# Kernel optimization log

Measured on AMD Instinct MI355X. Metric: run time of the kernel, lower is better.

Reference implementation:

```python
import jax, jax.numpy as jnp
import numpy as np
from jax import lax

BN_EPS = 1e-5
STRIDE = 1
PAD = 1  # autopad(3, d=1) = 1
DIL = 1
GROUPS = 1


def setup_inputs() -> dict:
    key = jax.random.key(0)
    ks = jax.random.split(key, 4)
    b, cin, h, w = 16, 256, 56, 56
    E, cout, k = 8, 256, 3
    x = jax.random.normal(ks[0], (b, cin, h, w), dtype=jnp.float32)
    routing_w = jax.random.normal(ks[1], (E, cin), dtype=jnp.float32) * (1.0 / np.sqrt(cin))
    routing_b = jax.random.normal(ks[2], (E,), dtype=jnp.float32) * 0.01
    # kaiming_normal fan_out: std = sqrt(2 / (cout * k * k))
    kw_std = np.sqrt(2.0 / (cout * k * k)).astype(np.float32)
    kernel_weights = jax.random.normal(ks[3], (E, cout, cin // GROUPS, k, k), dtype=jnp.float32) * kw_std
    bn_gamma = jnp.ones((cout,), dtype=jnp.float32)
    bn_beta = jnp.zeros((cout,), dtype=jnp.float32)
    bn_mean = jnp.zeros((cout,), dtype=jnp.float32)
    bn_var = jnp.ones((cout,), dtype=jnp.float32)
    return {"x": x, "routing_w": routing_w, "routing_b": routing_b,
            "kernel_weights": kernel_weights, "bn_gamma": bn_gamma,
            "bn_beta": bn_beta, "bn_mean": bn_mean, "bn_var": bn_var}


def reference(x, routing_w, routing_b, kernel_weights, bn_gamma, bn_beta, bn_mean, bn_var):
    # Routing: sigmoid(Linear(GAP(x)))  -> (b, E)
    pooled = x.mean(axis=(2, 3))                                   # (b, cin)
    r = jax.nn.sigmoid(pooled @ routing_w.T + routing_b)           # (b, E)
    # Per-sample combined kernels: sum_e r[b,e] * W[e]  -> (b, cout, cin, k, k)
    cw = jnp.einsum('be,eoihw->boihw', r, kernel_weights)
    # Per-sample conv (equivalent to the grouped conv with groups=b trick)
    def conv1(xi, wi):
        # xi: (cin, H, W), wi: (cout, cin, k, k)
        return lax.conv_general_dilated(
            xi[None], wi,
            window_strides=(STRIDE, STRIDE),
            padding=((PAD, PAD), (PAD, PAD)),
            rhs_dilation=(DIL, DIL),
            dimension_numbers=('NCHW', 'OIHW', 'NCHW'),
            feature_group_count=GROUPS)[0]
    y = jax.vmap(conv1)(x, cw)                                     # (b, cout, H, W)
    # BatchNorm (inference form) + SiLU
    inv = bn_gamma / jnp.sqrt(bn_var + BN_EPS)
    y = y * inv[None, :, None, None] + (bn_beta - bn_mean * inv)[None, :, None, None]
    return jax.nn.silu(y)
```

## Files before the change

kernel.cpp:

```cpp
#include <hip/hip_runtime.h>
#include <hip/hip_bf16.h>

typedef unsigned short u16;
typedef __attribute__((ext_vector_type(8))) short s16x8;
typedef __attribute__((ext_vector_type(4))) float f32x4;
typedef __attribute__((address_space(3))) u16 lds_u16;
typedef __attribute__((address_space(1))) const u16 g_u16;

#define CIN 256
#define COUT 256
#define NPIX 3136
#define CWROW 168
#define CWPB (16 * COUT * CWROW)

__device__ __forceinline__ u16 f2b(float f) {
  union { float f; unsigned u; } c; c.f = f;
  unsigned r = (c.u + 0x7FFFu + ((c.u >> 16) & 1u)) >> 16;
  return (u16)r;
}

__global__ __launch_bounds__(256)
void transpose_gap_kernel(const float* __restrict__ x, u16* __restrict__ xq,
                          float* __restrict__ pooled) {
  const int hg = blockIdx.x, ck = blockIdx.y, b = blockIdx.z;
  const int tid = threadIdx.x;
  const int ci = tid >> 4, sub = tid & 15;
  __shared__ __align__(16) u16 tile[928 * 8];

  if (tid < 32) {
    int r = tid >> 2, c4 = tid & 3;
    int u = r * 116 + (c4 < 2 ? c4 : 112 + c4);
    int us = u ^ ((u >> 3) & 7);
    *(uint4*)&tile[us * 8] = (uint4){0, 0, 0, 0};
  }

  const float* src = x + ((size_t)(b * CIN + ck * 16 + ci) * NPIX + (size_t)hg * 448);
  float s = 0.f;
#pragma unroll
  for (int it = 0; it < 7; ++it) {
    int p = it * 16 + sub;
    int row = p / 14, wq = p - row * 14;
    float4 v = *(const float4*)(src + p * 4);
    s += v.x + v.y + v.z + v.w;
    u16 q[4] = { f2b(v.x), f2b(v.y), f2b(v.z), f2b(v.w) };
#pragma unroll
    for (int k = 0; k < 4; ++k) {
      int wp = wq * 4 + 1 + k;
      int u = (row * 58 + wp) * 2 + (ci >> 3);
      int us = u ^ ((u >> 3) & 7);
      tile[us * 8 + (ci & 7)] = q[k];
    }
  }
  for (int off = 8; off; off >>= 1) s += __shfl_down(s, off, 16);
  if (sub == 0) atomicAdd(&pooled[b * CIN + ck * 16 + ci], s);

  __syncthreads();
  uint4* dst = (uint4*)(xq + ((size_t)(b * 16 + ck) * 58 + hg * 8 + 1) * 928);
  for (int idx = tid; idx < 928; idx += 256) {
    int us = idx ^ ((idx >> 3) & 7);
    dst[idx] = *(const uint4*)&tile[us * 8];
  }
  if (hg == 0 && tid < 116)
    ((uint4*)(xq + ((size_t)(b * 16 + ck) * 58) * 928))[tid] = (uint4){0, 0, 0, 0};
  if (hg == 6 && tid < 116)
    ((uint4*)(xq + ((size_t)(b * 16 + ck) * 58 + 57) * 928))[tid] = (uint4){0, 0, 0, 0};
}

__global__ __launch_bounds__(256)
void combine_kernel(const float* __restrict__ W, const float* __restrict__ pooled,
                    const float* __restrict__ rw, const float* __restrict__ rb,
                    u16* __restrict__ cw) {
  const int o = blockIdx.x, tid = threadIdx.x;
  __shared__ float rs[128];
  __shared__ __align__(16) u16 st[2][16 * CWROW];

  for (int i = tid; i < 672; i += 256) ((uint4*)st)[i] = (uint4){0, 0, 0, 0};

  if (tid < 128) {
    int b = tid >> 3, e = tid & 7;
    float s = rb[e];
    const float* pb = pooled + b * CIN;
    const float* we = rw + e * CIN;
    for (int c = 0; c < CIN; ++c) s += (pb[c] * (1.f / 3136.f)) * we[c];
    rs[tid] = 1.f / (1.f + __expf(-s));
  }
  float wreg[8][9];
#pragma unroll
  for (int e = 0; e < 8; ++e) {
    const float* wp = W + ((size_t)(e * COUT + o)) * 2304 + tid;
#pragma unroll
    for (int k = 0; k < 9; ++k) wreg[e][k] = wp[k * 256];
  }
  int slot[9];
#pragma unroll
  for (int k = 0; k < 9; ++k) {
    int j = tid + k * 256, ci = j / 9, t = j - ci * 9;
    slot[k] = (ci >> 4) * CWROW + t * 16 + (ci & 15);
  }
  __syncthreads();
  for (int b = 0; b < 16; ++b) {
    u16* sb = st[b & 1];
    float rv[8];
#pragma unroll
    for (int e = 0; e < 8; ++e) rv[e] = rs[b * 8 + e];
#pragma unroll
    for (int k = 0; k < 9; ++k) {
      float a = 0.f;
#pragma unroll
      for (int e = 0; e < 8; ++e) a += rv[e] * wreg[e][k];
      sb[slot[k]] = f2b(a);
    }
    __syncthreads();
    u16* dstb = cw + (size_t)b * CWPB;
    for (int i = tid; i < 336; i += 256) {
      int ck = i / 21, q = i - ck * 21;
      *(uint4*)(dstb + ck * (256 * CWROW) + o * CWROW + q * 8) =
          *(const uint4*)(sb + ck * CWROW + q * 8);
    }
  }
}

__global__ __launch_bounds__(256)
void conv_kernel(const u16* __restrict__ xq, const u16* __restrict__ cw,
                 const float* __restrict__ bng, const float* __restrict__ bnb,
                 const float* __restrict__ bnm, const float* __restrict__ bnv,
                 float* __restrict__ out) {
  const int l = blockIdx.x;
  const int xcd = l & 7, s = l >> 3;
  const int bb = (s >= 28) ? 1 : 0;
  const int b = xcd + 8 * bb;
  const int r = s - 28 * bb;
  const int ob = r / 7;
  const int o0 = ob * 64, h0 = (r - ob * 7) * 8;
  const int tid = threadIdx.x;
  const int wv = tid >> 6, lane = tid & 63, quad = lane >> 4, ln = lane & 15;

  __shared__ __align__(16) u16 xs[2][19 * 512];
  __shared__ __align__(16) u16 as_[2][64 * CWROW];

  f32x4 acc[4][7];
#pragma unroll
  for (int ms = 0; ms < 4; ++ms)
#pragma unroll
    for (int ns = 0; ns < 7; ++ns) acc[ms][ns] = (f32x4){0.f, 0.f, 0.f, 0.f};

  int bsite[7];
#pragma unroll
  for (int ns = 0; ns < 7; ++ns) {
    int pi = ns * 16 + ln;
    int hr = (pi >= 56) ? 1 : 0;
    int wc = pi - hr * 56;
    bsite[ns] = ((2 * wv + hr) * 58 + wc) * 16;
  }

  auto STAGE = [&](int ck, int buf) {
    const u16* xsrc = xq + ((size_t)(b * 16 + ck) * 58 + h0) * 928;
    const u16* asrc = cw + (size_t)b * CWPB + ((size_t)ck * COUT + o0) * CWROW;
    for (int g = wv; g < 40; g += 4) {
      if (g < 19)
        __builtin_amdgcn_global_load_lds((g_u16*)(xsrc + g * 512 + lane * 8),
                                         (lds_u16*)(&xs[buf][g * 512]), 16, 0, 0);
      else
        __builtin_amdgcn_global_load_lds((g_u16*)(asrc + (g - 19) * 512 + lane * 8),
                                         (lds_u16*)(&as_[buf][(g - 19) * 512]), 16, 0, 0);
    }
  };

  auto COMPUTE = [&](int buf) {
#pragma unroll
    for (int tp = 0; tp < 5; ++tp) {
      int t = tp * 2 + (quad >> 1);
      int dy, dx;
      if (t < 9) { dy = t / 3; dx = t - dy * 3; } else { dy = 1; dx = 1; }
      const int boff = (dy * 58 + dx) * 16 + (quad & 1) * 8;
      s16x8 af[4];
#pragma unroll
      for (int ms = 0; ms < 4; ++ms)
        af[ms] = *(const s16x8*)&as_[buf][(ms * 16 + ln) * CWROW + tp * 32 + quad * 8];
#pragma unroll
      for (int ns = 0; ns < 7; ++ns) {
        s16x8 bfr = *(const s16x8*)&xs[buf][bsite[ns] + boff];
#pragma unroll
        for (int ms = 0; ms < 4; ++ms)
          acc[ms][ns] = __builtin_amdgcn_mfma_f32_16x16x32_bf16(af[ms], bfr, acc[ms][ns], 0, 0, 0);
      }
    }
  };

  STAGE(0, 0);
  __syncthreads();
  for (int ck = 0; ck < 16; ck += 2) {
    STAGE(ck + 1, 1);
    COMPUTE(0);
    __syncthreads();
    if (ck < 14) STAGE(ck + 2, 0);
    COMPUTE(1);
    __syncthreads();
  }

#pragma unroll
  for (int ms = 0; ms < 4; ++ms) {
#pragma unroll
    for (int rr = 0; rr < 4; ++rr) {
      int o = o0 + ms * 16 + quad * 4 + rr;
      float inv = bng[o] * rsqrtf(bnv[o] + 1e-5f);
      float bias = bnb[o] - bnm[o] * inv;
      float* obp = out + ((size_t)(b * COUT + o)) * NPIX;
#pragma unroll
      for (int ns = 0; ns < 7; ++ns) {
        int pi = ns * 16 + ln;
        int hr = (pi >= 56) ? 1 : 0;
        int wc = pi - hr * 56;
        int hg = h0 + 2 * wv + hr;
        float v = acc[ms][ns][rr] * inv + bias;
        v = v / (1.f + __expf(-v));
        obp[hg * 56 + wc] = v;
      }
    }
  }
}

extern "C" void kernel_launch(void* const* d_in, const int* in_sizes, int n_in,
                              void* d_out, int out_size, void* d_ws, size_t ws_size,
                              hipStream_t stream) {
  const float* x   = (const float*)d_in[0];
  const float* rw  = (const float*)d_in[1];
  const float* rb  = (const float*)d_in[2];
  const float* W   = (const float*)d_in[3];
  const float* bng = (const float*)d_in[4];
  const float* bnb = (const float*)d_in[5];
  const float* bnm = (const float*)d_in[6];
  const float* bnv = (const float*)d_in[7];
  float* out = (float*)d_out;

  char* wsb = (char*)d_ws;
  u16*  cw     = (u16*)wsb;
  u16*  xq     = (u16*)(wsb + 22020096);
  float* pooled = (float*)(wsb + 22020096 + 27558912);

  hipMemsetAsync(pooled, 0, 16 * CIN * sizeof(float), stream);
  transpose_gap_kernel<<<dim3(7, 16, 16), 256, 0, stream>>>(x, xq, pooled);
  combine_kernel<<<256, 256, 0, stream>>>(W, pooled, rw, rb, cw);
  conv_kernel<<<dim3(448), 256, 0, stream>>>(xq, cw, bng, bnb, bnm, bnv, out);
}
```

Measured before the change: 233.4 us.

## Retile conv to 14-row blocks with triple-buffered pipeline and drop GAP atomics

The conv kernel now uses 256 blocks of 448 threads (7 waves), each covering 14 output rows and 64 output channels. It triple-buffers LDS stages with explicit vmcnt waits, raw barriers and raised MFMA priority, so loads are issued two chunks ahead. The GAP reduction writes per-row-group partial sums that combine_kernel adds up in LDS, which removes the atomics and the memset launch. Per-tap offsets are also hoisted out of the compute loop. The larger LDS footprint and single-block occupancy risk worse latency hiding.

```diff
diff --git a/kernel.cpp b/kernel.cpp
--- a/kernel.cpp
+++ b/kernel.cpp
@@ -21,7 +21,7 @@
 
 __global__ __launch_bounds__(256)
 void transpose_gap_kernel(const float* __restrict__ x, u16* __restrict__ xq,
-                          float* __restrict__ pooled) {
+                          float* __restrict__ parts) {
   const int hg = blockIdx.x, ck = blockIdx.y, b = blockIdx.z;
   const int tid = threadIdx.x;
   const int ci = tid >> 4, sub = tid & 15;
@@ -33,7 +33,6 @@
     int us = u ^ ((u >> 3) & 7);
     *(uint4*)&tile[us * 8] = (uint4){0, 0, 0, 0};
   }
-
   const float* src = x + ((size_t)(b * CIN + ck * 16 + ci) * NPIX + (size_t)hg * 448);
   float s = 0.f;
 #pragma unroll
@@ -52,8 +51,7 @@
     }
   }
   for (int off = 8; off; off >>= 1) s += __shfl_down(s, off, 16);
-  if (sub == 0) atomicAdd(&pooled[b * CIN + ck * 16 + ci], s);
-
+  if (sub == 0) parts[(hg * 16 + b) * 256 + ck * 16 + ci] = s;
   __syncthreads();
   uint4* dst = (uint4*)(xq + ((size_t)(b * 16 + ck) * 58 + hg * 8 + 1) * 928);
   for (int idx = tid; idx < 928; idx += 256) {
@@ -67,19 +65,26 @@
 }
 
 __global__ __launch_bounds__(256)
-void combine_kernel(const float* __restrict__ W, const float* __restrict__ pooled,
+void combine_kernel(const float* __restrict__ W, const float* __restrict__ parts,
                     const float* __restrict__ rw, const float* __restrict__ rb,
                     u16* __restrict__ cw) {
   const int o = blockIdx.x, tid = threadIdx.x;
+  __shared__ float pooled_lds[16 * 256];
   __shared__ float rs[128];
   __shared__ __align__(16) u16 st[2][16 * CWROW];
-
-  for (int i = tid; i < 672; i += 256) ((uint4*)st)[i] = (uint4){0, 0, 0, 0};
-
+  for (int b = 0; b < 16; ++b) {
+    float s = 0.f;
+#pragma unroll
+    for (int hg = 0; hg < 7; ++hg) s += parts[(hg * 16 + b) * 256 + tid];
+    pooled_lds[b * 256 + tid] = s;
+  }
+  for (int i = tid; i < (2 * 16 * CWROW) / 8; i += 256)
+    ((uint4*)st)[i] = (uint4){0, 0, 0, 0};
+  __syncthreads();
   if (tid < 128) {
     int b = tid >> 3, e = tid & 7;
     float s = rb[e];
-    const float* pb = pooled + b * CIN;
+    const float* pb = pooled_lds + b * 256;
     const float* we = rw + e * CIN;
     for (int c = 0; c < CIN; ++c) s += (pb[c] * (1.f / 3136.f)) * we[c];
     rs[tid] = 1.f / (1.f + __expf(-s));
@@ -120,23 +125,22 @@
   }
 }
 
-__global__ __launch_bounds__(256)
+__global__ __launch_bounds__(448, 1)
 void conv_kernel(const u16* __restrict__ xq, const u16* __restrict__ cw,
                  const float* __restrict__ bng, const float* __restrict__ bnb,
                  const float* __restrict__ bnm, const float* __restrict__ bnv,
                  float* __restrict__ out) {
   const int l = blockIdx.x;
   const int xcd = l & 7, s = l >> 3;
-  const int bb = (s >= 28) ? 1 : 0;
-  const int b = xcd + 8 * bb;
-  const int r = s - 28 * bb;
-  const int ob = r / 7;
-  const int o0 = ob * 64, h0 = (r - ob * 7) * 8;
+  const int b = 2 * xcd + (s >> 4);
+  const int rem = s & 15;
+  const int ob = rem >> 2, hb = rem & 3;
+  const int o0 = ob * 64, h0 = hb * 14;
   const int tid = threadIdx.x;
   const int wv = tid >> 6, lane = tid & 63, quad = lane >> 4, ln = lane & 15;
 
-  __shared__ __align__(16) u16 xs[2][19 * 512];
-  __shared__ __align__(16) u16 as_[2][64 * CWROW];
+  __shared__ __align__(16) u16 xs[3][14848];
+  __shared__ __align__(16) u16 as_[3][10752];
 
   f32x4 acc[4][7];
 #pragma unroll
@@ -152,34 +156,47 @@
     int wc = pi - hr * 56;
     bsite[ns] = ((2 * wv + hr) * 58 + wc) * 16;
   }
+  int boffp[5];
+#pragma unroll
+  for (int tp = 0; tp < 5; ++tp) {
+    int t = tp * 2 + (quad >> 1);
+    int dy, dx;
+    if (t < 9) { dy = t / 3; dx = t - dy * 3; } else { dy = 1; dx = 1; }
+    boffp[tp] = (dy * 58 + dx) * 16 + (quad & 1) * 8;
+  }
+  int abase[4];
+#pragma unroll
+  for (int ms = 0; ms < 4; ++ms) abase[ms] = (ms * 16 + ln) * CWROW + quad * 8;
+
+  const int g0 = (wv == 0) ? 0 : 8 + (wv - 1) * 7;
 
   auto STAGE = [&](int ck, int buf) {
     const u16* xsrc = xq + ((size_t)(b * 16 + ck) * 58 + h0) * 928;
     const u16* asrc = cw + (size_t)b * CWPB + ((size_t)ck * COUT + o0) * CWROW;
-    for (int g = wv; g < 40; g += 4) {
-      if (g < 19)
-        __builtin_amdgcn_global_load_lds((g_u16*)(xsrc + g * 512 + lane * 8),
-                                         (lds_u16*)(&xs[buf][g * 512]), 16, 0, 0);
-      else
-        __builtin_amdgcn_global_load_lds((g_u16*)(asrc + (g - 19) * 512 + lane * 8),
-                                         (lds_u16*)(&as_[buf][(g - 19) * 512]), 16, 0, 0);
+#pragma unroll
+    for (int i = 0; i < 8; ++i) {
+      if (i < 7 || wv == 0) {
+        int G = g0 + i;
+        if (G < 29)
+          __builtin_amdgcn_global_load_lds((g_u16*)(xsrc + G * 512 + lane * 8),
+                                           (lds_u16*)(&xs[buf][G * 512]), 16, 0, 0);
+        else
+          __builtin_amdgcn_global_load_lds((g_u16*)(asrc + (G - 29) * 512 + lane * 8),
+                                           (lds_u16*)(&as_[buf][(G - 29) * 512]), 16, 0, 0);
+      }
     }
   };
 
   auto COMPUTE = [&](int buf) {
 #pragma unroll
     for (int tp = 0; tp < 5; ++tp) {
-      int t = tp * 2 + (quad >> 1);
-      int dy, dx;
-      if (t < 9) { dy = t / 3; dx = t - dy * 3; } else { dy = 1; dx = 1; }
-      const int boff = (dy * 58 + dx) * 16 + (quad & 1) * 8;
       s16x8 af[4];
 #pragma unroll
       for (int ms = 0; ms < 4; ++ms)
-        af[ms] = *(const s16x8*)&as_[buf][(ms * 16 + ln) * CWROW + tp * 32 + quad * 8];
+        af[ms] = *(const s16x8*)&as_[buf][abase[ms] + tp * 32];
 #pragma unroll
       for (int ns = 0; ns < 7; ++ns) {
-        s16x8 bfr = *(const s16x8*)&xs[buf][bsite[ns] + boff];
+        s16x8 bfr = *(const s16x8*)&xs[buf][bsite[ns] + boffp[tp]];
 #pragma unroll
         for (int ms = 0; ms < 4; ++ms)
           acc[ms][ns] = __builtin_amdgcn_mfma_f32_16x16x32_bf16(af[ms], bfr, acc[ms][ns], 0, 0, 0);
@@ -188,15 +205,28 @@
   };
 
   STAGE(0, 0);
-  __syncthreads();
-  for (int ck = 0; ck < 16; ck += 2) {
-    STAGE(ck + 1, 1);
-    COMPUTE(0);
-    __syncthreads();
-    if (ck < 14) STAGE(ck + 2, 0);
-    COMPUTE(1);
-    __syncthreads();
-  }
+  STAGE(1, 1);
+#define CONV_WINDOW(CK, BUF, SBUF, DO_STAGE, LAST)                                  \
+  {                                                                                 \
+    if (LAST)            asm volatile("s_waitcnt vmcnt(0)" ::: "memory");           \
+    else if (wv == 0)    asm volatile("s_waitcnt vmcnt(8)" ::: "memory");           \
+    else                 asm volatile("s_waitcnt vmcnt(7)" ::: "memory");           \
+    __builtin_amdgcn_sched_barrier(0);                                              \
+    __builtin_amdgcn_s_barrier();                                                   \
+    __builtin_amdgcn_sched_barrier(0);                                              \
+    if (DO_STAGE) STAGE((CK) + 2, SBUF);                                            \
+    __builtin_amdgcn_s_setprio(1);                                                  \
+    COMPUTE(BUF);                                                                   \
+    __builtin_amdgcn_s_setprio(0);                                                  \
+  }
+  for (int jj = 0; jj < 5; ++jj) {
+    int ck = jj * 3;
+    CONV_WINDOW(ck,     0, 2, true,      false);
+    CONV_WINDOW(ck + 1, 1, 0, true,      false);
+    CONV_WINDOW(ck + 2, 2, 1, (jj < 4),  false);
+  }
+  CONV_WINDOW(15, 0, 0, false, true);
+#undef CONV_WINDOW
 
 #pragma unroll
   for (int ms = 0; ms < 4; ++ms) {
@@ -234,12 +264,11 @@
   float* out = (float*)d_out;
 
   char* wsb = (char*)d_ws;
-  u16*  cw     = (u16*)wsb;
-  u16*  xq     = (u16*)(wsb + 22020096);
-  float* pooled = (float*)(wsb + 22020096 + 27558912);
-
-  hipMemsetAsync(pooled, 0, 16 * CIN * sizeof(float), stream);
-  transpose_gap_kernel<<<dim3(7, 16, 16), 256, 0, stream>>>(x, xq, pooled);
-  combine_kernel<<<256, 256, 0, stream>>>(W, pooled, rw, rb, cw);
-  conv_kernel<<<dim3(448), 256, 0, stream>>>(xq, cw, bng, bnb, bnm, bnv, out);
-}
+  u16*  cw    = (u16*)wsb;
+  u16*  xq    = (u16*)(wsb + 22020096);
+  float* parts = (float*)(wsb + 22020096 + 27558912);
+
+  transpose_gap_kernel<<<dim3(7, 16, 16), 256, 0, stream>>>(x, xq, parts);
+  combine_kernel<<<256, 256, 0, stream>>>(W, parts, rw, rb, cw);
+  conv_kernel<<<dim3(256), 448, 0, stream>>>(xq, cw, bng, bnb, bnm, bnv, out);
+}
```

Measured after the change: 227.0 us. 1.03x faster.
